# Performance work log

Measured on AMD Instinct MI355X. Metric: run time of the kernel, lower is better.

Reference implementation:

```python
import jax, jax.numpy as jnp
import numpy as np

D = 1e-6
B, N, E, K = 128, 512, 512, 256


def _lower_median_abs(x, axis):
    # torch.median returns the LOWER of the two middle values for even counts
    n = x.shape[axis]
    s = jnp.sort(jnp.abs(x), axis=axis)
    return jnp.take(s, (n - 1) // 2, axis=axis)


def _bounds_from_cauchy(head, errors, k):
    # errors: (B, E, *head.shape[1:]); E divisible by k in this config
    b, e = errors.shape[0], errors.shape[1]
    tail = errors.shape[2:]
    chunks = errors.reshape(b, e // k, k, *tail)
    l1 = _lower_median_abs(chunks, axis=2).sum(axis=1)
    return head - l1, head + l1


def _relaxed_exp(h, errs, noise, lb, ub):
    is_tight = ub == lb
    lam_s = (jnp.exp(ub) - jnp.exp(lb)) / (ub - lb + D)
    lam = jnp.minimum(lam_s, jnp.exp(lb + 1.0 - 0.1))
    ub0 = jnp.where(lam > lam_s, jnp.exp(lb) - lam * lb, jnp.exp(ub) - lam * ub)
    mu = 0.5 * (lam * (1.0 - jnp.log(lam)) + ub0)
    delta = 0.5 * (ub0 - lam * (1.0 - jnp.log(lam)))
    lam = jnp.where(is_tight, 0.0, lam)
    mu = jnp.where(is_tight, jnp.exp(ub), mu)
    delta = jnp.where(is_tight, 0.0, delta)
    new_head = h * lam + mu
    new_errs = jnp.concatenate([errs * lam[:, None], delta[:, None] * noise], axis=1)
    return new_head, new_errs


def _relaxed_log(h, errs, noise, lb, ub):
    is_tight = ub == lb
    lam_s = (jnp.log(ub) - jnp.log(lb + D)) / (ub - lb + D)
    lam = lam_s
    lb0 = jnp.where(lam < lam_s, jnp.log(ub) - ub * lam, jnp.log(lb + D) - lb * lam)
    mu = 0.5 * (-jnp.log(lam) - 1.0 + lb0)
    delta = 0.5 * (-jnp.log(lam) - 1.0 - lb0)
    lam = jnp.where(is_tight, 0.0, lam)
    mu = jnp.where(is_tight, jnp.log(ub), mu)
    delta = jnp.where(is_tight, 0.0, delta)
    new_head = h * lam + mu
    new_errs = jnp.concatenate([errs * lam[:, None], delta[:, None] * noise], axis=1)
    return new_head, new_errs


def setup_inputs() -> dict:
    key = jax.random.key(0)
    k1, k2, k3, k4 = jax.random.split(key, 4)
    curr_head = jax.random.normal(k1, (B, N), dtype=jnp.float32)
    # small error magnitudes keep exp/log relaxation bounds valid (lb of log stage > 0)
    curr_errors = 1e-3 * jax.random.normal(k2, (B * E, N), dtype=jnp.float32)
    cauchy_exp = jax.random.cauchy(k3, (B, K, N), dtype=jnp.float32)
    cauchy_log = jax.random.cauchy(k4, (B, K), dtype=jnp.float32)
    return {"curr_head": curr_head, "curr_errors": curr_errors,
            "cauchy_exp": cauchy_exp, "cauchy_log": cauchy_log, "k": K}


def reference(curr_head, curr_errors, cauchy_exp, cauchy_log, k):
    b, n = curr_head.shape
    max_head = jax.lax.stop_gradient(jnp.max(curr_head, axis=1, keepdims=True))  # (B,1)
    temp_head = curr_head - max_head                         # (B,N)
    errs = curr_errors.reshape(b, -1, n)                     # (B,E,N)
    lb, ub = _bounds_from_cauchy(temp_head, errs, k)
    exp_head, exp_errs = _relaxed_exp(temp_head, errs, cauchy_exp, lb, ub)  # (B,N),(B,E+K,N)
    exp_head = exp_head.sum(axis=1)                          # (B,)
    exp_errs = exp_errs.sum(axis=2)                          # (B,E+K)
    lb2, ub2 = _bounds_from_cauchy(exp_head, exp_errs, k)
    ls_head, ls_errs = _relaxed_log(exp_head, exp_errs, cauchy_log, lb2, ub2)  # (B,),(B,E+2K)
    ls_head = ls_head + max_head[:, 0]
    return ls_head, ls_errs.reshape(-1)
```

## Files before the change

### kernel.cpp

```cpp
#include <hip/hip_runtime.h>
#include <cstdint>
#include <cstddef>

#define BB 128
#define NN 512
#define EE 512
#define KK 256
#define STR 17

__device__ __forceinline__ float wave_reduce_max(float v) {
#pragma unroll
  for (int off = 32; off >= 1; off >>= 1) v = fmaxf(v, __shfl_xor(v, off, 64));
  return v;
}
__device__ __forceinline__ float wave_reduce_sum(float v) {
#pragma unroll
  for (int off = 32; off >= 1; off >>= 1) v += __shfl_xor(v, off, 64);
  return v;
}

template <int CTRL>
__device__ __forceinline__ float dppz(float x) {
  return __int_as_float(__builtin_amdgcn_update_dpp(0, __float_as_int(x), CTRL, 0xf, 0xf, false));
}
template <int CTRL>
__device__ __forceinline__ float dppi(float x) {
  return __int_as_float(__builtin_amdgcn_update_dpp(__float_as_int(x), __float_as_int(x), CTRL, 0xf, 0xf, false));
}
__device__ __forceinline__ float wave_sum64(float x) {
  x += dppz<0x111>(x); x += dppz<0x112>(x); x += dppz<0x114>(x); x += dppz<0x118>(x);
  x += dppz<0x142>(x); x += dppz<0x143>(x);
  return __int_as_float(__builtin_amdgcn_readlane(__float_as_int(x), 63));
}
__device__ __forceinline__ float wave_max64nn(float x) {
  x = fmaxf(x, dppz<0x111>(x)); x = fmaxf(x, dppz<0x112>(x));
  x = fmaxf(x, dppz<0x114>(x)); x = fmaxf(x, dppz<0x118>(x));
  x = fmaxf(x, dppz<0x142>(x)); x = fmaxf(x, dppz<0x143>(x));
  return __int_as_float(__builtin_amdgcn_readlane(__float_as_int(x), 63));
}
__device__ __forceinline__ float wave_min64(float x) {
  x = fminf(x, dppi<0x111>(x)); x = fminf(x, dppi<0x112>(x));
  x = fminf(x, dppi<0x114>(x)); x = fminf(x, dppi<0x118>(x));
  x = fminf(x, dppi<0x142>(x)); x = fminf(x, dppi<0x143>(x));
  return __int_as_float(__builtin_amdgcn_readlane(__float_as_int(x), 63));
}

__device__ __forceinline__ float wave_median256_fast(float a0, float a1, float a2, float a3) {
  float S = wave_sum64((a0 + a1) + (a2 + a3));
  float mean = S * 0.00390625f;
  float lo = 0.f, hi = S * 1.0000002f + 1e-37f;
  int c_lo = 0, c_hi = 256;
  float piv = 0.845f * mean;
  float ans = 0.f;
  bool have = false;
#pragma unroll 1
  for (int it = 0; it < 34; ++it) {
    if (!(piv > lo && piv < hi)) piv = 0.5f * (lo + hi);
    int cnt = __popcll(__ballot(a0 < piv)) + __popcll(__ballot(a1 < piv)) +
              __popcll(__ballot(a2 < piv)) + __popcll(__ballot(a3 < piv));
    if (cnt == 128) {
      float m = fmaxf(fmaxf(a0 < piv ? a0 : 0.f, a1 < piv ? a1 : 0.f),
                      fmaxf(a2 < piv ? a2 : 0.f, a3 < piv ? a3 : 0.f));
      ans = wave_max64nn(m); have = true; break;
    }
    if (cnt == 127) {
      float m = fminf(fminf(a0 >= piv ? a0 : 3.4e38f, a1 >= piv ? a1 : 3.4e38f),
                      fminf(a2 >= piv ? a2 : 3.4e38f, a3 >= piv ? a3 : 3.4e38f));
      ans = wave_min64(m); have = true; break;
    }
    if (cnt < 127) { lo = piv; c_lo = cnt; } else { hi = piv; c_hi = cnt; }
    if (it == 0) piv = piv + (127.5f - (float)cnt) * mean * 0.0077f;
    else piv = lo + (hi - lo) * ((127.5f - (float)c_lo) / (float)(c_hi - c_lo));
    if (it >= 10) piv = 0.5f * (lo + hi);
  }
  if (!have) {
    float m = fmaxf(fmaxf(a0 < hi ? a0 : 0.f, a1 < hi ? a1 : 0.f),
                    fmaxf(a2 < hi ? a2 : 0.f, a3 < hi ? a3 : 0.f));
    ans = wave_max64nn(m);
  }
  return ans;
}

__global__ __launch_bounds__(256, 4) void kfused(
    const float* __restrict__ head, const float* __restrict__ errs,
    float* __restrict__ ws_delta, float* __restrict__ ws_htpart,
    float* __restrict__ ws_epart) {
  __shared__ float tile[512 * STR];
  __shared__ float medbuf[32];
  __shared__ float lambuf[16];
  __shared__ float redm[4];
  const int blk = blockIdx.x;
  const int b = blk >> 5, g = blk & 31;
  const int n0 = g * 16;
  const int tid = threadIdx.x, wave = tid >> 6, lane = tid & 63;

  float m = fmaxf(head[(size_t)b * NN + tid], head[(size_t)b * NN + 256 + tid]);
  m = wave_reduce_max(m);
  if (lane == 0) redm[wave] = m;

  const int tr = tid >> 2, tc = (tid & 3) * 4;
  const float* src = errs + (size_t)b * EE * NN + n0 + tc;
#pragma unroll
  for (int i = 0; i < 8; ++i) {
    int row = i * 64 + tr;
    float4 v = *(const float4*)(src + (size_t)row * NN);
    float* dst = &tile[row * STR + tc];
    dst[0] = v.x; dst[1] = v.y; dst[2] = v.z; dst[3] = v.w;
  }
  __syncthreads();
  float hmax = fmaxf(fmaxf(redm[0], redm[1]), fmaxf(redm[2], redm[3]));

#pragma unroll 1
  for (int j = 0; j < 8; ++j) {
    int p = wave * 8 + j;
    int col = p & 15;
    int rb = (p >> 4) * 256;
    float a0 = fabsf(tile[(rb + lane) * STR + col]);
    float a1 = fabsf(tile[(rb + lane + 64) * STR + col]);
    float a2 = fabsf(tile[(rb + lane + 128) * STR + col]);
    float a3 = fabsf(tile[(rb + lane + 192) * STR + col]);
    float med = wave_median256_fast(a0, a1, a2, a3);
    if (lane == 0) medbuf[p] = med;
  }
  __syncthreads();

  float htp = 0.f;
  if (tid < 16) {
    int n = n0 + tid;
    float l1 = medbuf[tid] + medbuf[16 + tid];
    float th = head[(size_t)b * NN + n] - hmax;
    float lb = th - l1, ub = th + l1;
    float lam, mu, delta;
    if (ub == lb) {
      lam = 0.f; mu = expf(ub); delta = 0.f;
    } else {
      float elb = expf(lb), eub = expf(ub);
      float lam_s = (eub - elb) / (ub - lb + 1e-6f);
      lam = fminf(lam_s, expf(lb + 0.9f));
      float ub0 = (lam > lam_s) ? (elb - lam * lb) : (eub - lam * ub);
      float t = lam * (1.f - logf(lam));
      mu = 0.5f * (t + ub0);
      delta = 0.5f * (ub0 - t);
    }
    lambuf[tid] = lam;
    ws_delta[(size_t)b * NN + n] = delta;
    htp = th * lam + mu;
  }
  if (wave == 0) {
    float s = wave_reduce_sum(htp);
    if (lane == 0) ws_htpart[b * 32 + g] = s;
  }
  __syncthreads();

  float s0 = 0.f, s1 = 0.f;
#pragma unroll
  for (int j = 0; j < 16; ++j) {
    float w = lambuf[j];
    s0 = fmaf(tile[tid * STR + j], w, s0);
    s1 = fmaf(tile[(tid + 256) * STR + j], w, s1);
  }
  float* op = ws_epart + ((size_t)(b * 32 + g)) * 512;
  op[tid] = s0;
  op[tid + 256] = s1;
}

__global__ __launch_bounds__(256) void kcexp(
    const float* __restrict__ cexp, const float* __restrict__ ws_delta,
    float* __restrict__ ws_ee2) {
  const int blk = blockIdx.x;
  const int b = blk >> 2, part = blk & 3;
  const int wave = threadIdx.x >> 6, lane = threadIdx.x & 63;
  const float* wsrc = ws_delta + (size_t)b * NN;
  float4 wa = *(const float4*)(wsrc + 4 * lane);
  float4 wb = *(const float4*)(wsrc + 256 + 4 * lane);
  const int r0 = part * 64 + wave * 16;
  const float* base = cexp + (size_t)b * KK * NN;
  float* out = ws_ee2 + (size_t)b * KK;
#pragma unroll 1
  for (int i = 0; i < 16; ++i) {
    int r = r0 + i;
    const float* rp = base + (size_t)r * NN;
    float4 x = *(const float4*)(rp + 4 * lane);
    float4 y = *(const float4*)(rp + 256 + 4 * lane);
    float s = x.x * wa.x + x.y * wa.y + x.z * wa.z + x.w * wa.w +
              y.x * wb.x + y.y * wb.y + y.z * wb.z + y.w * wb.w;
    s = wave_reduce_sum(s);
    if (lane == 0) out[r] = s;
  }
}

__global__ __launch_bounds__(256) void kstage3(
    const float* __restrict__ head, const float* __restrict__ clog,
    const float* __restrict__ ws_htpart, const float* __restrict__ ws_epart,
    const float* __restrict__ ws_ee2, float* __restrict__ out) {
  __shared__ float eb[768];
  __shared__ float redm[4];
  __shared__ float meds[3];
  __shared__ float sc[2];
  __shared__ float ehsh;
  const int b = blockIdx.x;
  const int tid = threadIdx.x, wave = tid >> 6, lane = tid & 63;

  float m = fmaxf(head[(size_t)b * NN + tid], head[(size_t)b * NN + 256 + tid]);
  m = wave_reduce_max(m);
  if (lane == 0) redm[wave] = m;

  float acc0 = 0.f, acc1 = 0.f;
  const float* pp = ws_epart + (size_t)b * 32 * 512;
#pragma unroll
  for (int g = 0; g < 32; ++g) {
    acc0 += pp[g * 512 + tid];
    acc1 += pp[g * 512 + 256 + tid];
  }
  eb[tid] = acc0;
  eb[tid + 256] = acc1;
  eb[tid + 512] = ws_ee2[(size_t)b * KK + tid];
  __syncthreads();

  if (wave < 3) {
    const float* p = eb + wave * 256;
    float a0 = fabsf(p[lane]), a1 = fabsf(p[lane + 64]);
    float a2 = fabsf(p[lane + 128]), a3 = fabsf(p[lane + 192]);
    float med = wave_median256_fast(a0, a1, a2, a3);
    if (lane == 0) meds[wave] = med;
  } else {
    float v = (lane < 32) ? ws_htpart[b * 32 + lane] : 0.f;
    v = wave_reduce_sum(v);
    if (lane == 0) ehsh = v;
  }
  __syncthreads();

  if (tid == 0) {
    float hmax = fmaxf(fmaxf(redm[0], redm[1]), fmaxf(redm[2], redm[3]));
    float eh = ehsh;
    float l1 = meds[0] + meds[1] + meds[2];
    float lb = eh - l1, ub = eh + l1;
    float lam, mu, delta;
    if (ub == lb) {
      lam = 0.f; mu = logf(ub); delta = 0.f;
    } else {
      float llb = logf(lb + 1e-6f);
      float lam_s = (logf(ub) - llb) / (ub - lb + 1e-6f);
      lam = lam_s;
      float lb0 = llb - lb * lam;
      float t = -logf(lam) - 1.f;
      mu = 0.5f * (t + lb0);
      delta = 0.5f * (t - lb0);
    }
    sc[0] = lam; sc[1] = delta;
    out[b] = eh * lam + mu + hmax;
  }
  __syncthreads();
  float lam = sc[0], delta = sc[1];
  float* ob = out + BB + (size_t)b * 1024;
  ob[tid] = eb[tid] * lam;
  ob[tid + 256] = eb[tid + 256] * lam;
  ob[tid + 512] = eb[tid + 512] * lam;
  ob[tid + 768] = delta * clog[(size_t)b * KK + tid];
}

extern "C" void kernel_launch(void* const* d_in, const int* in_sizes, int n_in,
                              void* d_out, int out_size, void* d_ws, size_t ws_size,
                              hipStream_t stream) {
  const float* head = (const float*)d_in[0];
  const float* errs = (const float*)d_in[1];
  const float* cexp = (const float*)d_in[2];
  const float* clog = (const float*)d_in[3];
  float* out = (float*)d_out;

  float* ws = (float*)d_ws;
  float* ws_delta = ws;
  float* ws_htpart = ws_delta + BB * NN;
  float* ws_ee2 = ws_htpart + BB * 32;
  float* ws_epart = ws_ee2 + BB * KK;

  hipLaunchKernelGGL(kfused, dim3(BB * 32), dim3(256), 0, stream,
                     head, errs, ws_delta, ws_htpart, ws_epart);
  hipLaunchKernelGGL(kcexp, dim3(BB * 4), dim3(256), 0, stream,
                     cexp, ws_delta, ws_ee2);
  hipLaunchKernelGGL(kstage3, dim3(BB), dim3(256), 0, stream,
                     head, clog, ws_htpart, ws_epart, ws_ee2, out);
}
```

Before: 270.0 us.

## Widen fused block to 512 threads, split cexp rows, add separate partial-reduce kernel

The main fused kernel now uses 512 threads per block, so each thread loads fewer tile rows and computes fewer medians. The cexp dot-product kernel uses four times as many blocks, each wave handling four rows with independent loads issued before the reductions. The per-block partial sums are now reduced in a new kernel spread across 256 blocks instead of inside the 128-block final stage. This adds one more launch and a small extra workspace round trip, and the larger block may limit occupancy.

```diff
diff --git a/kernel.cpp b/kernel.cpp
--- a/kernel.cpp
+++ b/kernel.cpp
@@ -81,38 +81,37 @@
   return ans;
 }
 
-__global__ __launch_bounds__(256, 4) void kfused(
+__global__ __launch_bounds__(512, 8) void kfused(
     const float* __restrict__ head, const float* __restrict__ errs,
     float* __restrict__ ws_delta, float* __restrict__ ws_htpart,
     float* __restrict__ ws_epart) {
   __shared__ float tile[512 * STR];
   __shared__ float medbuf[32];
   __shared__ float lambuf[16];
-  __shared__ float redm[4];
+  __shared__ float redm[8];
   const int blk = blockIdx.x;
   const int b = blk >> 5, g = blk & 31;
   const int n0 = g * 16;
   const int tid = threadIdx.x, wave = tid >> 6, lane = tid & 63;
 
-  float m = fmaxf(head[(size_t)b * NN + tid], head[(size_t)b * NN + 256 + tid]);
+  float m = head[(size_t)b * NN + tid];
   m = wave_reduce_max(m);
   if (lane == 0) redm[wave] = m;
 
   const int tr = tid >> 2, tc = (tid & 3) * 4;
   const float* src = errs + (size_t)b * EE * NN + n0 + tc;
 #pragma unroll
-  for (int i = 0; i < 8; ++i) {
-    int row = i * 64 + tr;
+  for (int i = 0; i < 4; ++i) {
+    int row = i * 128 + tr;
     float4 v = *(const float4*)(src + (size_t)row * NN);
     float* dst = &tile[row * STR + tc];
     dst[0] = v.x; dst[1] = v.y; dst[2] = v.z; dst[3] = v.w;
   }
   __syncthreads();
-  float hmax = fmaxf(fmaxf(redm[0], redm[1]), fmaxf(redm[2], redm[3]));
 
 #pragma unroll 1
-  for (int j = 0; j < 8; ++j) {
-    int p = wave * 8 + j;
+  for (int j = 0; j < 4; ++j) {
+    int p = wave * 4 + j;
     int col = p & 15;
     int rb = (p >> 4) * 256;
     float a0 = fabsf(tile[(rb + lane) * STR + col]);
@@ -126,6 +125,8 @@
 
   float htp = 0.f;
   if (tid < 16) {
+    float hmax = fmaxf(fmaxf(fmaxf(redm[0], redm[1]), fmaxf(redm[2], redm[3])),
+                       fmaxf(fmaxf(redm[4], redm[5]), fmaxf(redm[6], redm[7])));
     int n = n0 + tid;
     float l1 = medbuf[tid] + medbuf[16 + tid];
     float th = head[(size_t)b * NN + n] - hmax;
@@ -152,46 +153,76 @@
   }
   __syncthreads();
 
-  float s0 = 0.f, s1 = 0.f;
-#pragma unroll
-  for (int j = 0; j < 16; ++j) {
-    float w = lambuf[j];
-    s0 = fmaf(tile[tid * STR + j], w, s0);
-    s1 = fmaf(tile[(tid + 256) * STR + j], w, s1);
-  }
-  float* op = ws_epart + ((size_t)(b * 32 + g)) * 512;
-  op[tid] = s0;
-  op[tid + 256] = s1;
+  float s0 = 0.f;
+#pragma unroll
+  for (int j = 0; j < 16; ++j) s0 = fmaf(tile[tid * STR + j], lambuf[j], s0);
+  ws_epart[((size_t)(b * 32 + g)) * 512 + tid] = s0;
 }
 
 __global__ __launch_bounds__(256) void kcexp(
     const float* __restrict__ cexp, const float* __restrict__ ws_delta,
     float* __restrict__ ws_ee2) {
   const int blk = blockIdx.x;
-  const int b = blk >> 2, part = blk & 3;
+  const int b = blk >> 4, seg = blk & 15;
   const int wave = threadIdx.x >> 6, lane = threadIdx.x & 63;
   const float* wsrc = ws_delta + (size_t)b * NN;
   float4 wa = *(const float4*)(wsrc + 4 * lane);
   float4 wb = *(const float4*)(wsrc + 256 + 4 * lane);
-  const int r0 = part * 64 + wave * 16;
+  const int r0 = seg * 16 + wave * 4;
   const float* base = cexp + (size_t)b * KK * NN;
   float* out = ws_ee2 + (size_t)b * KK;
-#pragma unroll 1
-  for (int i = 0; i < 16; ++i) {
-    int r = r0 + i;
-    const float* rp = base + (size_t)r * NN;
+  float s0, s1, s2, s3;
+  {
+    const float* rp = base + (size_t)r0 * NN;
     float4 x = *(const float4*)(rp + 4 * lane);
     float4 y = *(const float4*)(rp + 256 + 4 * lane);
-    float s = x.x * wa.x + x.y * wa.y + x.z * wa.z + x.w * wa.w +
-              y.x * wb.x + y.y * wb.y + y.z * wb.z + y.w * wb.w;
-    s = wave_reduce_sum(s);
-    if (lane == 0) out[r] = s;
-  }
+    s0 = x.x * wa.x + x.y * wa.y + x.z * wa.z + x.w * wa.w +
+         y.x * wb.x + y.y * wb.y + y.z * wb.z + y.w * wb.w;
+  }
+  {
+    const float* rp = base + (size_t)(r0 + 1) * NN;
+    float4 x = *(const float4*)(rp + 4 * lane);
+    float4 y = *(const float4*)(rp + 256 + 4 * lane);
+    s1 = x.x * wa.x + x.y * wa.y + x.z * wa.z + x.w * wa.w +
+         y.x * wb.x + y.y * wb.y + y.z * wb.z + y.w * wb.w;
+  }
+  {
+    const float* rp = base + (size_t)(r0 + 2) * NN;
+    float4 x = *(const float4*)(rp + 4 * lane);
+    float4 y = *(const float4*)(rp + 256 + 4 * lane);
+    s2 = x.x * wa.x + x.y * wa.y + x.z * wa.z + x.w * wa.w +
+         y.x * wb.x + y.y * wb.y + y.z * wb.z + y.w * wb.w;
+  }
+  {
+    const float* rp = base + (size_t)(r0 + 3) * NN;
+    float4 x = *(const float4*)(rp + 4 * lane);
+    float4 y = *(const float4*)(rp + 256 + 4 * lane);
+    s3 = x.x * wa.x + x.y * wa.y + x.z * wa.z + x.w * wa.w +
+         y.x * wb.x + y.y * wb.y + y.z * wb.z + y.w * wb.w;
+  }
+  s0 = wave_sum64(s0);
+  s1 = wave_sum64(s1);
+  s2 = wave_sum64(s2);
+  s3 = wave_sum64(s3);
+  if (lane == 0) {
+    out[r0] = s0; out[r0 + 1] = s1; out[r0 + 2] = s2; out[r0 + 3] = s3;
+  }
+}
+
+__global__ __launch_bounds__(256) void kreduce(
+    const float* __restrict__ ws_epart, float* __restrict__ ws_ee1) {
+  const int idx = blockIdx.x * 256 + threadIdx.x;
+  const int b = idx >> 9, e = idx & 511;
+  const float* pp = ws_epart + (size_t)b * 32 * 512 + e;
+  float acc = 0.f;
+#pragma unroll
+  for (int g = 0; g < 32; ++g) acc += pp[g * 512];
+  ws_ee1[idx] = acc;
 }
 
 __global__ __launch_bounds__(256) void kstage3(
     const float* __restrict__ head, const float* __restrict__ clog,
-    const float* __restrict__ ws_htpart, const float* __restrict__ ws_epart,
+    const float* __restrict__ ws_htpart, const float* __restrict__ ws_ee1,
     const float* __restrict__ ws_ee2, float* __restrict__ out) {
   __shared__ float eb[768];
   __shared__ float redm[4];
@@ -205,15 +236,8 @@
   m = wave_reduce_max(m);
   if (lane == 0) redm[wave] = m;
 
-  float acc0 = 0.f, acc1 = 0.f;
-  const float* pp = ws_epart + (size_t)b * 32 * 512;
-#pragma unroll
-  for (int g = 0; g < 32; ++g) {
-    acc0 += pp[g * 512 + tid];
-    acc1 += pp[g * 512 + 256 + tid];
-  }
-  eb[tid] = acc0;
-  eb[tid + 256] = acc1;
+  eb[tid] = ws_ee1[(size_t)b * NN + tid];
+  eb[tid + 256] = ws_ee1[(size_t)b * NN + 256 + tid];
   eb[tid + 512] = ws_ee2[(size_t)b * KK + tid];
   __syncthreads();
 
@@ -272,12 +296,15 @@
   float* ws_delta = ws;
   float* ws_htpart = ws_delta + BB * NN;
   float* ws_ee2 = ws_htpart + BB * 32;
-  float* ws_epart = ws_ee2 + BB * KK;
-
-  hipLaunchKernelGGL(kfused, dim3(BB * 32), dim3(256), 0, stream,
+  float* ws_ee1 = ws_ee2 + BB * KK;
+  float* ws_epart = ws_ee1 + BB * NN;
+
+  hipLaunchKernelGGL(kfused, dim3(BB * 32), dim3(512), 0, stream,
                      head, errs, ws_delta, ws_htpart, ws_epart);
-  hipLaunchKernelGGL(kcexp, dim3(BB * 4), dim3(256), 0, stream,
+  hipLaunchKernelGGL(kcexp, dim3(BB * 16), dim3(256), 0, stream,
                      cexp, ws_delta, ws_ee2);
+  hipLaunchKernelGGL(kreduce, dim3(256), dim3(256), 0, stream,
+                     ws_epart, ws_ee1);
   hipLaunchKernelGGL(kstage3, dim3(BB), dim3(256), 0, stream,
-                     head, clog, ws_htpart, ws_epart, ws_ee2, out);
-}
+                     head, clog, ws_htpart, ws_ee1, ws_ee2, out);
+}
```

Result: no change. 265.2 us (-1.8%).
